# Kernel tuning notes

Hardware: AMD Instinct MI355X
Metric: run time of the kernel (lower is better)

The kernel has to match this reference:

```python
import jax, jax.numpy as jnp
import numpy as np

B, L, D = 4, 64, 512          # batch, trajectory length, d_model
DI, N, DC, R = 1024, 16, 4, 32  # d_inner, d_state, d_conv, dt_rank
NL = 4                         # n_layers
SD, AD, MEL = 17, 6, 1000      # state_dim, act_dim, max_ep_len
EPS = 1e-5


def setup_inputs() -> dict:
    key = jax.random.key(0)
    ks = iter(jax.random.split(key, 40))
    nrm = lambda shp, s=0.02: jax.random.normal(next(ks), shp, jnp.float32) * s
    inp = {
        "states": jax.random.normal(next(ks), (B, L, SD), jnp.float32),
        "actions": jax.random.normal(next(ks), (B, L, AD), jnp.float32),
        "returns_to_go": jax.random.normal(next(ks), (B, L, 1), jnp.float32),
        "constraints_to_go": jax.random.normal(next(ks), (B, L, 1), jnp.float32),
        "timesteps": jax.random.randint(next(ks), (B, L), 0, MEL, jnp.int32),
        # embedding / projection heads (torch Linear: y = x @ W.T + b)
        "es_w": nrm((D, SD)), "es_b": jnp.zeros((D,), jnp.float32),
        "ea_w": nrm((D, AD)), "ea_b": jnp.zeros((D,), jnp.float32),
        "er_w": nrm((D, 1)), "er_b": jnp.zeros((D,), jnp.float32),
        "ec_w": nrm((D, 1)), "ec_b": jnp.zeros((D,), jnp.float32),
        "et_w": nrm((MEL, D)),
        # per-layer Mamba params, stacked on leading NL axis
        "ln_w": jnp.ones((NL, D), jnp.float32), "ln_b": jnp.zeros((NL, D), jnp.float32),
        "in_w": nrm((NL, 2 * DI, D)),
        "conv_w": nrm((NL, DI, DC), 0.1), "conv_b": jnp.zeros((NL, DI), jnp.float32),
        "xp_w": nrm((NL, R + 2 * N, DI)),
        "dtp_w": nrm((NL, DI, R), 0.1),
        "dtp_b": jnp.full((NL, DI), -4.6, jnp.float32) + nrm((NL, DI), 0.1),
        "A_log": jnp.broadcast_to(jnp.log(jnp.arange(1, N + 1, dtype=jnp.float32)), (NL, DI, N)) * jnp.ones((NL, DI, 1), jnp.float32),
        "Dp": jnp.ones((NL, DI), jnp.float32),
        "out_w": nrm((NL, D, DI)),
        # final norm + heads
        "fn_w": jnp.ones((D,), jnp.float32), "fn_b": jnp.zeros((D,), jnp.float32),
        "ps_w": nrm((SD, D)), "ps_b": jnp.zeros((SD,), jnp.float32),
        "pa_w": nrm((AD, D)), "pa_b": jnp.zeros((AD,), jnp.float32),
    }
    return inp


def layernorm(x, w, b):
    mu = jnp.mean(x, -1, keepdims=True)
    var = jnp.mean(jnp.square(x - mu), -1, keepdims=True)
    return (x - mu) * jax.lax.rsqrt(var + EPS) * w + b


def selective_scan(u, delta, A, Bm, Cm, Dp):
    # u, delta: (B,T,DI); A: (DI,N); Bm, Cm: (B,T,N); Dp: (DI,)
    dA = jnp.exp(delta[..., None] * A)                      # (B,T,DI,N)
    dBu = delta[..., None] * Bm[:, :, None, :] * u[..., None]

    def step(h, xs):
        dA_t, dBu_t, C_t = xs
        h = dA_t * h + dBu_t                                # (B,DI,N)
        y = jnp.einsum('bdn,bn->bd', h, C_t)
        return h, y

    h0 = jnp.zeros((u.shape[0], u.shape[2], A.shape[1]), u.dtype)
    xs = (dA.transpose(1, 0, 2, 3), dBu.transpose(1, 0, 2, 3), Cm.transpose(1, 0, 2))
    _, ys = jax.lax.scan(step, h0, xs)
    return ys.transpose(1, 0, 2) + u * Dp


def mamba_mixer(x, in_w, conv_w, conv_b, xp_w, dtp_w, dtp_b, A_log, Dp, out_w):
    T = x.shape[1]
    xz = x @ in_w.T                                         # (B,T,2*DI)
    xm, z = jnp.split(xz, 2, axis=-1)
    # causal depthwise conv1d, kernel DC
    xpad = jnp.pad(xm, ((0, 0), (DC - 1, 0), (0, 0)))
    xc = sum(xpad[:, k:k + T, :] * conv_w[:, k] for k in range(DC)) + conv_b
    xc = jax.nn.silu(xc)
    dbc = xc @ xp_w.T                                       # (B,T,R+2N)
    dt, Bm, Cm = jnp.split(dbc, [R, R + N], axis=-1)
    delta = jax.nn.softplus(dt @ dtp_w.T + dtp_b)           # (B,T,DI)
    y = selective_scan(xc, delta, -jnp.exp(A_log), Bm, Cm, Dp)
    y = y * jax.nn.silu(z)
    return y @ out_w.T


def reference(states, actions, returns_to_go, constraints_to_go, timesteps,
              es_w, es_b, ea_w, ea_b, er_w, er_b, ec_w, ec_b, et_w,
              ln_w, ln_b, in_w, conv_w, conv_b, xp_w, dtp_w, dtp_b, A_log, Dp, out_w,
              fn_w, fn_b, ps_w, ps_b, pa_w, pa_b):
    te = et_w[timesteps]                                    # (B,L,D)
    se = states @ es_w.T + es_b + te
    ae = actions @ ea_w.T + ea_b + te
    re = returns_to_go @ er_w.T + er_b + te
    ce = constraints_to_go @ ec_w.T + ec_b + te
    # interleave (r, c, s, a) per timestep -> (B, 4L, D)
    x = jnp.stack((re, ce, se, ae), axis=2).reshape(B, 4 * L, D)
    for i in range(NL):
        x = x + mamba_mixer(layernorm(x, ln_w[i], ln_b[i]),
                            in_w[i], conv_w[i], conv_b[i], xp_w[i],
                            dtp_w[i], dtp_b[i], A_log[i], Dp[i], out_w[i])
    x = layernorm(x, fn_w, fn_b)
    outputs = x.reshape(B, L, 4, D).transpose(0, 2, 1, 3)   # (B,4,L,D)
    state_preds = outputs[:, 3] @ ps_w.T + ps_b             # from action tokens
    action_preds = outputs[:, 2] @ pa_w.T + pa_b            # from state tokens
    return state_preds, action_preds
```

## Files before the change

kernel.cpp:

```cpp
#include <hip/hip_runtime.h>
#include <math.h>

#define B_ 4
#define L_ 64
#define D_ 512
#define DI_ 1024
#define N_ 16
#define DC_ 4
#define R_ 32
#define NL_ 4
#define SD_ 17
#define AD_ 6
#define T_ 256
#define CH3_ 32
#define TC3_ 8
#define DL3_ 8

#define NW_IN  (NL_ * 2 * DI_ * D_)
#define NW_OUT (NL_ * D_ * DI_)
#define NW_XP  (NL_ * 64 * DI_)
#define NW_TOT (NW_IN + NW_OUT + NW_XP)
#define WCVT_BLOCKS (NW_TOT / 4 / 256)

typedef short bf16x8 __attribute__((ext_vector_type(8)));
typedef float f32x4 __attribute__((ext_vector_type(4)));

__device__ __forceinline__ float silu_f(float v) { return v / (1.f + __expf(-v)); }
__device__ __forceinline__ float softplus_f(float v) {
    return fmaxf(v, 0.f) + log1pf(__expf(-fabsf(v)));
}
__device__ __forceinline__ unsigned short f2bs(float f) {
    unsigned u = __float_as_uint(f);
    u += 0x7fffu + ((u >> 16) & 1u);
    return (unsigned short)(u >> 16);
}
__device__ __forceinline__ float bs2f(unsigned short s) {
    return __uint_as_float(((unsigned)s) << 16);
}

__global__ __launch_bounds__(256) void init_kernel(
    const float* __restrict__ in_w, const float* __restrict__ out_w,
    const float* __restrict__ xp_w, unsigned short* __restrict__ wb,
    const float* __restrict__ states, const float* __restrict__ actions,
    const float* __restrict__ rtg, const float* __restrict__ ctg,
    const int* __restrict__ ts,
    const float* __restrict__ es_w, const float* __restrict__ es_b,
    const float* __restrict__ ea_w, const float* __restrict__ ea_b,
    const float* __restrict__ er_w, const float* __restrict__ er_b,
    const float* __restrict__ ec_w, const float* __restrict__ ec_b,
    const float* __restrict__ et_w, float* __restrict__ x)
{
    if (blockIdx.x < WCVT_BLOCKS) {
        const int i = blockIdx.x * 256 + threadIdx.x;
        const int e = i * 4;
        const float* src; int off;
        if (e < NW_IN)               { src = in_w;  off = e; }
        else if (e < NW_IN + NW_OUT) { src = out_w; off = e - NW_IN; }
        else                         { src = xp_w;  off = e - NW_IN - NW_OUT; }
        const float4 v = *(const float4*)(src + off);
        ushort4 o;
        o.x = f2bs(v.x); o.y = f2bs(v.y); o.z = f2bs(v.z); o.w = f2bs(v.w);
        *(ushort4*)(wb + e) = o;
    } else {
        const int bl = blockIdx.x - WCVT_BLOCKS;
#pragma unroll
        for (int j = 0; j < 2; ++j) {
            const int d = threadIdx.x + j * 256;
            const float te = et_w[(size_t)ts[bl] * D_ + d];
            const float r = rtg[bl] * er_w[d] + er_b[d] + te;
            const float c = ctg[bl] * ec_w[d] + ec_b[d] + te;
            float s = es_b[d] + te;
#pragma unroll
            for (int k = 0; k < SD_; ++k) s += states[bl * SD_ + k] * es_w[d * SD_ + k];
            float a = ea_b[d] + te;
#pragma unroll
            for (int k = 0; k < AD_; ++k) a += actions[bl * AD_ + k] * ea_w[d * AD_ + k];
            float* xp = x + (size_t)bl * 4 * D_;
            xp[0 * D_ + d] = r;
            xp[1 * D_ + d] = c;
            xp[2 * D_ + d] = s;
            xp[3 * D_ + d] = a;
        }
    }
}

template <bool BF16OUT>
__global__ __launch_bounds__(256) void ln_kernel(
    const float* __restrict__ x, const float* __restrict__ w,
    const float* __restrict__ b, void* __restrict__ o_)
{
    const int tok = blockIdx.x;
    const int tid = threadIdx.x;
    const float2 v = reinterpret_cast<const float2*>(x + (size_t)tok * D_)[tid];
    float s = v.x + v.y;
#pragma unroll
    for (int off = 1; off < 64; off <<= 1) s += __shfl_xor(s, off);
    __shared__ float red[8];
    const int wv = tid >> 6;
    if ((tid & 63) == 0) red[wv] = s;
    __syncthreads();
    const float mean = (red[0] + red[1] + red[2] + red[3]) * (1.f / D_);
    const float dx = v.x - mean, dy = v.y - mean;
    float q = dx * dx + dy * dy;
#pragma unroll
    for (int off = 1; off < 64; off <<= 1) q += __shfl_xor(q, off);
    if ((tid & 63) == 0) red[4 + wv] = q;
    __syncthreads();
    const float var = (red[4] + red[5] + red[6] + red[7]) * (1.f / D_);
    const float r = rsqrtf(var + 1e-5f);
    const int d0 = tid * 2;
    const float o0 = dx * r * w[d0] + b[d0];
    const float o1 = dy * r * w[d0 + 1] + b[d0 + 1];
    if (BF16OUT) {
        unsigned short* o = (unsigned short*)o_;
        o[(size_t)tok * D_ + d0] = f2bs(o0);
        o[(size_t)tok * D_ + d0 + 1] = f2bs(o1);
    } else {
        float* o = (float*)o_;
        o[(size_t)tok * D_ + d0] = o0;
        o[(size_t)tok * D_ + d0 + 1] = o1;
    }
}

__global__ __launch_bounds__(256) void inproj_kernel(
    const unsigned short* __restrict__ A, const unsigned short* __restrict__ W,
    const float* __restrict__ cw, const float* __restrict__ cb,
    unsigned short* __restrict__ xcb, unsigned short* __restrict__ zs)
{
    __shared__ unsigned short sxm[80][72];
    const int lane = threadIdx.x & 63, wid = threadIdx.x >> 6;
    const int r = lane & 15, kq = lane >> 4;
    const int m0 = blockIdx.y * 64;
    const int n0 = blockIdx.x * 64;
    const bool is_xm = (n0 < DI_);
    const int wm = m0 + (wid >> 1) * 32;
    const int wn = n0 + (wid & 1) * 32;
    f32x4 acc[2][2] = {};
    f32x4 accx[2] = {};
    int xrow = m0 - 16 + r;
    if (xrow < 0) xrow = 0;
#pragma unroll 4
    for (int k0 = 0; k0 < D_; k0 += 32) {
        bf16x8 a[2], b[2];
#pragma unroll
        for (int i = 0; i < 2; ++i)
            a[i] = *(const bf16x8*)(A + (size_t)(wm + i * 16 + r) * D_ + k0 + kq * 8);
#pragma unroll
        for (int j = 0; j < 2; ++j)
            b[j] = *(const bf16x8*)(W + (size_t)(wn + j * 16 + r) * D_ + k0 + kq * 8);
#pragma unroll
        for (int i = 0; i < 2; ++i)
#pragma unroll
            for (int j = 0; j < 2; ++j)
                acc[i][j] = __builtin_amdgcn_mfma_f32_16x16x32_bf16(a[i], b[j], acc[i][j], 0, 0, 0);
        if (is_xm) {
            const bf16x8 ax = *(const bf16x8*)(A + (size_t)xrow * D_ + k0 + kq * 8);
#pragma unroll
            for (int j = 0; j < 2; ++j)
                accx[j] = __builtin_amdgcn_mfma_f32_16x16x32_bf16(ax, b[j], accx[j], 0, 0, 0);
        }
    }
    if (!is_xm) {
#pragma unroll
        for (int i = 0; i < 2; ++i)
#pragma unroll
            for (int j = 0; j < 2; ++j)
#pragma unroll
                for (int g = 0; g < 4; ++g) {
                    const int row = wm + i * 16 + kq * 4 + g;
                    const int col = wn + j * 16 + r - DI_;
                    zs[(size_t)row * DI_ + col] = f2bs(silu_f(acc[i][j][g]));
                }
        return;
    }
#pragma unroll
    for (int i = 0; i < 2; ++i)
#pragma unroll
        for (int j = 0; j < 2; ++j)
#pragma unroll
            for (int g = 0; g < 4; ++g) {
                const int srow = 16 + (wm - m0) + i * 16 + kq * 4 + g;
                const int scol = (wn - n0) + j * 16 + r;
                sxm[srow][scol] = f2bs(acc[i][j][g]);
            }
#pragma unroll
    for (int j = 0; j < 2; ++j)
#pragma unroll
        for (int g = 0; g < 4; ++g) {
            const int srow = kq * 4 + g;
            const int scol = (wn - n0) + j * 16 + r;
            sxm[srow][scol] = f2bs(accx[j][g]);
        }
    __syncthreads();
    for (int e = threadIdx.x; e < 64 * 64; e += 256) {
        const int col = e & 63, rrel = e >> 6;
        const int grow = m0 + rrel;
        const int t = grow & (T_ - 1);
        const int d = n0 + col;
        const float4 w4 = ((const float4*)cw)[d];
        float a = cb[d];
#pragma unroll
        for (int k = 0; k < DC_; ++k) {
            if (t - 3 + k >= 0) {
                const float wk = (k == 0) ? w4.x : (k == 1) ? w4.y
                               : (k == 2) ? w4.z : w4.w;
                a += wk * bs2f(sxm[16 + rrel - 3 + k][col]);
            }
        }
        xcb[(size_t)grow * DI_ + d] = f2bs(silu_f(a));
    }
}

__global__ __launch_bounds__(256) void xp_kernel(
    const unsigned short* __restrict__ xcb, const unsigned short* __restrict__ Wb,
    float* __restrict__ dbc)
{
    __shared__ float red[4][16][64];
    const int tid = threadIdx.x;
    const int wid = tid >> 6, lane = tid & 63;
    const int r = lane & 15, kq = lane >> 4;
    const int m0 = blockIdx.x * 16;
    f32x4 acc4[4] = {};
    const int k00 = wid * 256;
#pragma unroll
    for (int ks = 0; ks < 8; ++ks) {
        const int k0 = k00 + ks * 32;
        const bf16x8 a = *(const bf16x8*)(xcb + (size_t)(m0 + r) * DI_ + k0 + kq * 8);
#pragma unroll
        for (int j = 0; j < 4; ++j) {
            const bf16x8 bfr = *(const bf16x8*)(Wb + (size_t)(j * 16 + r) * DI_ + k0 + kq * 8);
            acc4[j] = __builtin_amdgcn_mfma_f32_16x16x32_bf16(a, bfr, acc4[j], 0, 0, 0);
        }
    }
#pragma unroll
    for (int j = 0; j < 4; ++j)
#pragma unroll
        for (int g = 0; g < 4; ++g)
            red[wid][kq * 4 + g][j * 16 + r] = acc4[j][g];
    __syncthreads();
    for (int i = tid; i < 1024; i += 256) {
        const int row = i >> 6, col = i & 63;
        const float s = red[0][row][col] + red[1][row][col] +
                        red[2][row][col] + red[3][row][col];
        dbc[(size_t)(m0 + row) * 64 + col] = s;
    }
}

__global__ __launch_bounds__(256, 3) void scan_kernel(
    const unsigned short* __restrict__ xcb, const float* __restrict__ dbc,
    const float* __restrict__ dtw, const float* __restrict__ dtbias,
    const float* __restrict__ A_log, const float* __restrict__ Dp,
    const unsigned short* __restrict__ zs, unsigned short* __restrict__ ygb)
{
    __shared__ float dlt_s[T_][DL3_ + 1];
    __shared__ float Sl[CH3_][DL3_][17];
    __shared__ float Pl[CH3_][DL3_][17];
    const int tid = threadIdx.x;
    const int dl = tid & (DL3_ - 1);
    const int c = tid >> 3;
    const int b = blockIdx.x >> 7;
    const int d = (blockIdx.x & 127) * DL3_ + dl;
    const int row0 = b * T_ + c * TC3_;
    {
        const float4* Wp = (const float4*)(dtw + (size_t)d * R_);
        float4 w4[8];
#pragma unroll
        for (int q = 0; q < 8; ++q) w4[q] = Wp[q];
        const float bias = dtbias[d];
#pragma unroll
        for (int t = 0; t < TC3_; ++t) {
            const float4* Ap = (const float4*)(dbc + (size_t)(row0 + t) * 64);
            float acc = bias;
#pragma unroll
            for (int q = 0; q < 8; ++q) {
                const float4 a4 = Ap[q];
                acc += a4.x * w4[q].x + a4.y * w4[q].y + a4.z * w4[q].z + a4.w * w4[q].w;
            }
            dlt_s[c * TC3_ + t][dl] = softplus_f(acc);
        }
    }
    float Av[N_];
    {
        const float4* Alp = (const float4*)(A_log + (size_t)d * N_);
#pragma unroll
        for (int q = 0; q < 4; ++q) {
            const float4 v = Alp[q];
            Av[q * 4 + 0] = -__expf(v.x);
            Av[q * 4 + 1] = -__expf(v.y);
            Av[q * 4 + 2] = -__expf(v.z);
            Av[q * 4 + 3] = -__expf(v.w);
        }
    }
    __syncthreads();
    const unsigned short* up = xcb + (size_t)row0 * DI_ + d;
    const float* bc = dbc + (size_t)row0 * 64;
    float h[N_];
#pragma unroll
    for (int n = 0; n < N_; ++n) h[n] = 0.f;
    float dsum = 0.f;
#pragma unroll
    for (int t = 0; t < TC3_; ++t) {
        const float dt_t = dlt_s[c * TC3_ + t][dl];
        dsum += dt_t;
        const float dbu = dt_t * bs2f(up[t * DI_]);
#pragma unroll
        for (int q = 0; q < 4; ++q) {
            const float4 b4 = *(const float4*)(bc + t * 64 + R_ + q * 4);
            h[q * 4 + 0] = __expf(dt_t * Av[q * 4 + 0]) * h[q * 4 + 0] + dbu * b4.x;
            h[q * 4 + 1] = __expf(dt_t * Av[q * 4 + 1]) * h[q * 4 + 1] + dbu * b4.y;
            h[q * 4 + 2] = __expf(dt_t * Av[q * 4 + 2]) * h[q * 4 + 2] + dbu * b4.z;
            h[q * 4 + 3] = __expf(dt_t * Av[q * 4 + 3]) * h[q * 4 + 3] + dbu * b4.w;
        }
    }
#pragma unroll
    for (int n = 0; n < N_; ++n) {
        Sl[c][dl][n] = h[n];
        Pl[c][dl][n] = __expf(Av[n] * dsum);
    }
    __syncthreads();
    if (tid < DL3_ * N_) {
        const int dd = tid >> 4, nn = tid & 15;
        float hin = 0.f;
#pragma unroll
        for (int c2 = 0; c2 < CH3_; ++c2) {
            const float t2 = Pl[c2][dd][nn] * hin + Sl[c2][dd][nn];
            Sl[c2][dd][nn] = hin;
            hin = t2;
        }
    }
    __syncthreads();
#pragma unroll
    for (int n = 0; n < N_; ++n) h[n] = Sl[c][dl][n];
    const float Dd = Dp[d];
    const unsigned short* zp = zs + (size_t)row0 * DI_ + d;
    unsigned short* yp = ygb + (size_t)row0 * DI_ + d;
#pragma unroll
    for (int t = 0; t < TC3_; ++t) {
        const float dt_t = dlt_s[c * TC3_ + t][dl];
        const float ut = bs2f(up[t * DI_]);
        const float dbu = dt_t * ut;
        float y = ut * Dd;
#pragma unroll
        for (int q = 0; q < 4; ++q) {
            const float4 b4 = *(const float4*)(bc + t * 64 + R_ + q * 4);
            const float4 c4 = *(const float4*)(bc + t * 64 + R_ + N_ + q * 4);
            h[q * 4 + 0] = __expf(dt_t * Av[q * 4 + 0]) * h[q * 4 + 0] + dbu * b4.x;
            h[q * 4 + 1] = __expf(dt_t * Av[q * 4 + 1]) * h[q * 4 + 1] + dbu * b4.y;
            h[q * 4 + 2] = __expf(dt_t * Av[q * 4 + 2]) * h[q * 4 + 2] + dbu * b4.z;
            h[q * 4 + 3] = __expf(dt_t * Av[q * 4 + 3]) * h[q * 4 + 3] + dbu * b4.w;
            y += h[q * 4 + 0] * c4.x + h[q * 4 + 1] * c4.y
               + h[q * 4 + 2] * c4.z + h[q * 4 + 3] * c4.w;
        }
        yp[t * DI_] = f2bs(y * bs2f(zp[t * DI_]));
    }
}

__global__ __launch_bounds__(256) void outproj_kernel(
    const unsigned short* __restrict__ A, const unsigned short* __restrict__ W,
    float* __restrict__ x)
{
    const int lane = threadIdx.x & 63, w = threadIdx.x >> 6;
    const int r = lane & 15, kq = lane >> 4;
    const int m0 = blockIdx.y * 16;
    const int wn = blockIdx.x * 64 + w * 16;
    f32x4 acc = {};
#pragma unroll 4
    for (int k0 = 0; k0 < DI_; k0 += 32) {
        const bf16x8 a = *(const bf16x8*)(A + (size_t)(m0 + r) * DI_ + k0 + kq * 8);
        const bf16x8 b = *(const bf16x8*)(W + (size_t)(wn + r) * DI_ + k0 + kq * 8);
        acc = __builtin_amdgcn_mfma_f32_16x16x32_bf16(a, b, acc, 0, 0, 0);
    }
#pragma unroll
    for (int g = 0; g < 4; ++g) {
        const int row = m0 + kq * 4 + g;
        const int col = wn + r;
        x[(size_t)row * D_ + col] += acc[g];
    }
}

__global__ __launch_bounds__(256) void heads_kernel(
    const float* __restrict__ xn,
    const float* __restrict__ ps_w, const float* __restrict__ ps_b,
    const float* __restrict__ pa_w, const float* __restrict__ pa_b,
    float* __restrict__ out)
{
    const int idx = blockIdx.x * 4 + (threadIdx.x >> 6);
    const int lane = threadIdx.x & 63;
    const int bl = idx / 23, j = idx % 23;
    const float* tok;
    const float* wrow;
    float bias;
    float* dst;
    if (j < SD_) {
        tok = xn + ((size_t)bl * 4 + 3) * D_;
        wrow = ps_w + (size_t)j * D_;
        bias = ps_b[j];
        dst = out + (size_t)bl * SD_ + j;
    } else {
        const int jj = j - SD_;
        tok = xn + ((size_t)bl * 4 + 2) * D_;
        wrow = pa_w + (size_t)jj * D_;
        bias = pa_b[jj];
        dst = out + (size_t)B_ * L_ * SD_ + (size_t)bl * AD_ + jj;
    }
    float s = 0.f;
    for (int dd = lane; dd < D_; dd += 64) s += tok[dd] * wrow[dd];
#pragma unroll
    for (int off = 1; off < 64; off <<= 1) s += __shfl_xor(s, off);
    if (lane == 0) *dst = s + bias;
}

extern "C" void kernel_launch(void* const* d_in, const int* in_sizes, int n_in,
                              void* d_out, int out_size, void* d_ws, size_t ws_size,
                              hipStream_t stream)
{
    const float* states  = (const float*)d_in[0];
    const float* actions = (const float*)d_in[1];
    const float* rtg     = (const float*)d_in[2];
    const float* ctg     = (const float*)d_in[3];
    const int*   ts      = (const int*)d_in[4];
    const float* es_w = (const float*)d_in[5];  const float* es_b = (const float*)d_in[6];
    const float* ea_w = (const float*)d_in[7];  const float* ea_b = (const float*)d_in[8];
    const float* er_w = (const float*)d_in[9];  const float* er_b = (const float*)d_in[10];
    const float* ec_w = (const float*)d_in[11]; const float* ec_b = (const float*)d_in[12];
    const float* et_w = (const float*)d_in[13];
    const float* ln_w = (const float*)d_in[14]; const float* ln_b = (const float*)d_in[15];
    const float* in_w = (const float*)d_in[16];
    const float* conv_w = (const float*)d_in[17]; const float* conv_b = (const float*)d_in[18];
    const float* xp_w = (const float*)d_in[19];
    const float* dtp_w = (const float*)d_in[20]; const float* dtp_b = (const float*)d_in[21];
    const float* A_log = (const float*)d_in[22]; const float* Dp = (const float*)d_in[23];
    const float* out_w = (const float*)d_in[24];
    const float* fn_w = (const float*)d_in[25]; const float* fn_b = (const float*)d_in[26];
    const float* ps_w = (const float*)d_in[27]; const float* ps_b = (const float*)d_in[28];
    const float* pa_w = (const float*)d_in[29]; const float* pa_b = (const float*)d_in[30];
    float* out = (float*)d_out;

    float* ws   = (float*)d_ws;
    float* x    = ws;
    float* xn   = x + 524288;
    float* dbc  = xn + 524288;
    unsigned short* xnb = (unsigned short*)(dbc + 65536);
    unsigned short* xcb = xnb + 524288;
    unsigned short* zs  = xcb + 1048576;
    unsigned short* ygb = zs + 1048576;
    unsigned short* wb  = ygb + 1048576;
    unsigned short* wb_in  = wb;
    unsigned short* wb_out = wb + NW_IN;
    unsigned short* wb_xp  = wb + NW_IN + NW_OUT;

    init_kernel<<<WCVT_BLOCKS + B_ * L_, 256, 0, stream>>>(
        in_w, out_w, xp_w, wb,
        states, actions, rtg, ctg, ts,
        es_w, es_b, ea_w, ea_b, er_w, er_b, ec_w, ec_b, et_w, x);

    for (int i = 0; i < NL_; ++i) {
        ln_kernel<true><<<B_ * T_, 256, 0, stream>>>(
            x, ln_w + i * D_, ln_b + i * D_, xnb);
        inproj_kernel<<<dim3(32, 16), 256, 0, stream>>>(
            xnb, wb_in + (size_t)i * 2 * DI_ * D_,
            conv_w + i * DI_ * DC_, conv_b + i * DI_, xcb, zs);
        xp_kernel<<<64, 256, 0, stream>>>(
            xcb, wb_xp + (size_t)i * 64 * DI_, dbc);
        scan_kernel<<<B_ * (DI_ / DL3_), 256, 0, stream>>>(
            xcb, dbc, dtp_w + (size_t)i * DI_ * R_, dtp_b + i * DI_,
            A_log + (size_t)i * DI_ * N_, Dp + i * DI_, zs, ygb);
        outproj_kernel<<<dim3(8, 64), 256, 0, stream>>>(
            ygb, wb_out + (size_t)i * D_ * DI_, x);
    }

    ln_kernel<false><<<B_ * T_, 256, 0, stream>>>(x, fn_w, fn_b, xn);
    heads_kernel<<<(B_ * L_ * 23) / 4, 256, 0, stream>>>(xn, ps_w, ps_b, pa_w, pa_b, out);
}
```

Measured before the change: 310.4 us.

## Split-K out-projection with 2x2 MFMA tiles, fuse residual add into layernorm

The out-projection now gives each wave a 32x32 tile (2x2 MFMA fragments) instead of a 16x16 one. The K dimension is split in two across blockIdx.z, and each half writes its partial sum to a workspace buffer instead of doing a read-modify-write on x. The following layernorm kernel adds both partials into the residual stream, writes x back, and then normalizes. This aims for better operand reuse and enough blocks to fill the GPU while removing the separate residual update, at the cost of extra partial-buffer traffic.

```diff
diff --git a/kernel.cpp b/kernel.cpp
--- a/kernel.cpp
+++ b/kernel.cpp
@@ -84,14 +84,23 @@
     }
 }
 
-template <bool BF16OUT>
-__global__ __launch_bounds__(256) void ln_kernel(
-    const float* __restrict__ x, const float* __restrict__ w,
-    const float* __restrict__ b, void* __restrict__ o_)
+template <int MODE>
+__global__ __launch_bounds__(256) void ln2_kernel(
+    float* __restrict__ x, const float* __restrict__ p0,
+    const float* __restrict__ p1,
+    const float* __restrict__ w, const float* __restrict__ b,
+    void* __restrict__ o_)
 {
     const int tok = blockIdx.x;
     const int tid = threadIdx.x;
-    const float2 v = reinterpret_cast<const float2*>(x + (size_t)tok * D_)[tid];
+    float2 v = reinterpret_cast<float2*>(x + (size_t)tok * D_)[tid];
+    if (MODE >= 1) {
+        const float2 a0 = reinterpret_cast<const float2*>(p0 + (size_t)tok * D_)[tid];
+        const float2 a1 = reinterpret_cast<const float2*>(p1 + (size_t)tok * D_)[tid];
+        v.x += a0.x + a1.x;
+        v.y += a0.y + a1.y;
+        reinterpret_cast<float2*>(x + (size_t)tok * D_)[tid] = v;
+    }
     float s = v.x + v.y;
 #pragma unroll
     for (int off = 1; off < 64; off <<= 1) s += __shfl_xor(s, off);
@@ -111,14 +120,14 @@
     const int d0 = tid * 2;
     const float o0 = dx * r * w[d0] + b[d0];
     const float o1 = dy * r * w[d0 + 1] + b[d0 + 1];
-    if (BF16OUT) {
+    if (MODE == 2) {
+        float* o = (float*)o_;
+        o[(size_t)tok * D_ + d0] = o0;
+        o[(size_t)tok * D_ + d0 + 1] = o1;
+    } else {
         unsigned short* o = (unsigned short*)o_;
         o[(size_t)tok * D_ + d0] = f2bs(o0);
         o[(size_t)tok * D_ + d0 + 1] = f2bs(o1);
-    } else {
-        float* o = (float*)o_;
-        o[(size_t)tok * D_ + d0] = o0;
-        o[(size_t)tok * D_ + d0 + 1] = o1;
     }
 }
 
@@ -357,25 +366,39 @@
 
 __global__ __launch_bounds__(256) void outproj_kernel(
     const unsigned short* __restrict__ A, const unsigned short* __restrict__ W,
-    float* __restrict__ x)
-{
-    const int lane = threadIdx.x & 63, w = threadIdx.x >> 6;
+    float* __restrict__ p)
+{
+    const int lane = threadIdx.x & 63, wid = threadIdx.x >> 6;
     const int r = lane & 15, kq = lane >> 4;
-    const int m0 = blockIdx.y * 16;
-    const int wn = blockIdx.x * 64 + w * 16;
-    f32x4 acc = {};
+    const int wm = blockIdx.y * 64 + (wid >> 1) * 32;
+    const int wn = blockIdx.x * 64 + (wid & 1) * 32;
+    const int kb = blockIdx.z * 512;
+    f32x4 acc[2][2] = {};
 #pragma unroll 4
-    for (int k0 = 0; k0 < DI_; k0 += 32) {
-        const bf16x8 a = *(const bf16x8*)(A + (size_t)(m0 + r) * DI_ + k0 + kq * 8);
-        const bf16x8 b = *(const bf16x8*)(W + (size_t)(wn + r) * DI_ + k0 + kq * 8);
-        acc = __builtin_amdgcn_mfma_f32_16x16x32_bf16(a, b, acc, 0, 0, 0);
-    }
-#pragma unroll
-    for (int g = 0; g < 4; ++g) {
-        const int row = m0 + kq * 4 + g;
-        const int col = wn + r;
-        x[(size_t)row * D_ + col] += acc[g];
-    }
+    for (int k0 = 0; k0 < 512; k0 += 32) {
+        bf16x8 a[2], b[2];
+#pragma unroll
+        for (int i = 0; i < 2; ++i)
+            a[i] = *(const bf16x8*)(A + (size_t)(wm + i * 16 + r) * DI_ + kb + k0 + kq * 8);
+#pragma unroll
+        for (int j = 0; j < 2; ++j)
+            b[j] = *(const bf16x8*)(W + (size_t)(wn + j * 16 + r) * DI_ + kb + k0 + kq * 8);
+#pragma unroll
+        for (int i = 0; i < 2; ++i)
+#pragma unroll
+            for (int j = 0; j < 2; ++j)
+                acc[i][j] = __builtin_amdgcn_mfma_f32_16x16x32_bf16(a[i], b[j], acc[i][j], 0, 0, 0);
+    }
+#pragma unroll
+    for (int i = 0; i < 2; ++i)
+#pragma unroll
+        for (int j = 0; j < 2; ++j)
+#pragma unroll
+            for (int g = 0; g < 4; ++g) {
+                const int row = wm + i * 16 + kq * 4 + g;
+                const int col = wn + j * 16 + r;
+                p[(size_t)blockIdx.z * (1024 * 512) + (size_t)row * 512 + col] = acc[i][j][g];
+            }
 }
 
 __global__ __launch_bounds__(256) void heads_kernel(
@@ -439,7 +462,8 @@
     float* ws   = (float*)d_ws;
     float* x    = ws;
     float* xn   = x + 524288;
-    float* dbc  = xn + 524288;
+    float* p    = xn + 524288;
+    float* dbc  = p + 1048576;
     unsigned short* xnb = (unsigned short*)(dbc + 65536);
     unsigned short* xcb = xnb + 524288;
     unsigned short* zs  = xcb + 1048576;
@@ -455,8 +479,12 @@
         es_w, es_b, ea_w, ea_b, er_w, er_b, ec_w, ec_b, et_w, x);
 
     for (int i = 0; i < NL_; ++i) {
-        ln_kernel<true><<<B_ * T_, 256, 0, stream>>>(
-            x, ln_w + i * D_, ln_b + i * D_, xnb);
+        if (i == 0)
+            ln2_kernel<0><<<B_ * T_, 256, 0, stream>>>(
+                x, nullptr, nullptr, ln_w, ln_b, xnb);
+        else
+            ln2_kernel<1><<<B_ * T_, 256, 0, stream>>>(
+                x, p, p + 524288, ln_w + i * D_, ln_b + i * D_, xnb);
         inproj_kernel<<<dim3(32, 16), 256, 0, stream>>>(
             xnb, wb_in + (size_t)i * 2 * DI_ * D_,
             conv_w + i * DI_ * DC_, conv_b + i * DI_, xcb, zs);
@@ -465,10 +493,10 @@
         scan_kernel<<<B_ * (DI_ / DL3_), 256, 0, stream>>>(
             xcb, dbc, dtp_w + (size_t)i * DI_ * R_, dtp_b + i * DI_,
             A_log + (size_t)i * DI_ * N_, Dp + i * DI_, zs, ygb);
-        outproj_kernel<<<dim3(8, 64), 256, 0, stream>>>(
-            ygb, wb_out + (size_t)i * D_ * DI_, x);
-    }
-
-    ln_kernel<false><<<B_ * T_, 256, 0, stream>>>(x, fn_w, fn_b, xn);
+        outproj_kernel<<<dim3(8, 16, 2), 256, 0, stream>>>(
+            ygb, wb_out + (size_t)i * D_ * DI_, p);
+    }
+
+    ln2_kernel<2><<<B_ * T_, 256, 0, stream>>>(x, p, p + 524288, fn_w, fn_b, xn);
     heads_kernel<<<(B_ * L_ * 23) / 4, 256, 0, stream>>>(xn, ps_w, ps_b, pa_w, pa_b, out);
 }
```

After: 287.3 us (median of 2 runs). -7.4%, faster.
